# Kernel optimization log

Measured on AMD Instinct MI355X. Metric: run time of the kernel, lower is better.

The kernel has to match this reference:

```python
import jax, jax.numpy as jnp
import numpy as np

MAX_REL = 16  # max_relative_position (keys == values)


def _relative_positions(T, max_pos):
    r = jnp.arange(T)
    dist = r[None, :] - r[:, None]          # [T, T], k - q
    return jnp.clip(dist, -max_pos, max_pos) + max_pos


def setup_inputs() -> dict:
    key = jax.random.key(0)
    ks = jax.random.split(key, 5)
    B, H, T, D = 4, 16, 1024, 64
    V = 2 * MAX_REL + 1
    return {
        "q": jax.random.normal(ks[0], (B, H, T, D), jnp.float32),
        "k": jax.random.normal(ks[1], (B, H, T, D), jnp.float32),
        "v": jax.random.normal(ks[2], (B, H, T, D), jnp.float32),
        "emb_k": jax.random.normal(ks[3], (V, D), jnp.float32),
        "emb_v": jax.random.normal(ks[4], (V, D), jnp.float32),
    }


def reference(q, k, v, emb_k, emb_v):
    # q,k,v: [B,H,T,D]; emb_*: [2*MAX_REL+1, D]
    T = q.shape[2]
    D = k.shape[-1]
    rel_idx = _relative_positions(T, MAX_REL)          # [T,T]
    rel_k = emb_k[rel_idx]                             # [T,T,D]
    rel_v = emb_v[rel_idx]                             # [T,T,D]

    # content-content + content-position logits
    logits = jnp.einsum('bhtd,bhsd->bhts', q, k)
    logits = logits + jnp.einsum('bhtd,tsd->bhts', q, rel_k)
    logits = logits * (1.0 / jnp.sqrt(jnp.float32(D)))

    attn = jax.nn.softmax(logits, axis=-1)             # [B,H,T,T]
    out = jnp.einsum('bhts,bhsd->bhtd', attn, v)
    out = out + jnp.einsum('bhts,tsd->bhtd', attn, rel_v)
    return out, attn
```

## Files before the change

kernel.cpp:

```cpp
#include <hip/hip_runtime.h>
#include <hip/hip_bf16.h>

#define TT 1024
#define DD 64
#define MAXREL 16
#define NV 33
#define QBLK 16
#define SCALE 0.125f
#define BH 64

typedef short bf16x8 __attribute__((ext_vector_type(8)));
typedef short bf16x4 __attribute__((ext_vector_type(4)));
typedef float f32x4 __attribute__((ext_vector_type(4)));

#define SBAR() __builtin_amdgcn_sched_barrier(0)
#define WAITV(N)   __builtin_amdgcn_s_waitcnt(0x0F70 | (N))
#define WAITLGKM() __builtin_amdgcn_s_waitcnt(0xC07F)

static __device__ inline void gload16(const void* g, void* l) {
    __builtin_amdgcn_global_load_lds(
        (const __attribute__((address_space(1))) void*)g,
        (__attribute__((address_space(3))) void*)l, 16, 0, 0);
}

static __device__ inline short f2bf(float f) {
    __hip_bfloat16 h = __float2bfloat16(f);
    return *(short*)&h;
}
static __device__ inline float bf2f(short s) {
    union { unsigned u; float f; } x;
    x.u = ((unsigned)(unsigned short)s) << 16;
    return x.f;
}
static __device__ inline bf16x8 pack8(float4 a, float4 b) {
    bf16x8 r;
    r[0]=f2bf(a.x); r[1]=f2bf(a.y); r[2]=f2bf(a.z); r[3]=f2bf(a.w);
    r[4]=f2bf(b.x); r[5]=f2bf(b.y); r[6]=f2bf(b.z); r[7]=f2bf(b.w);
    return r;
}

__global__ __launch_bounds__(256)
void convk_kernel(const float* __restrict__ src, short* __restrict__ dst) {
    size_t i = (size_t)blockIdx.x * 256 + threadIdx.x;
    const float4* s = (const float4*)(src + i * 8);
    *(bf16x8*)(dst + i * 8) = pack8(s[0], s[1]);
}

__global__ __launch_bounds__(256)
void transv_kernel(const float* __restrict__ v, short* __restrict__ vt) {
    int bh = blockIdx.x >> 4;
    int st = blockIdx.x & 15;
    int wave = threadIdx.x >> 6, lane = threadIdx.x & 63;
    int s0 = st * 64 + wave * 16;
    const float* vp = v + ((size_t)bh * TT + s0) * DD + lane;
    bf16x8 lo, hi;
    #pragma unroll
    for (int e = 0; e < 8; ++e) lo[e] = f2bf(vp[(size_t)e * DD]);
    #pragma unroll
    for (int e = 0; e < 8; ++e) hi[e] = f2bf(vp[(size_t)(e + 8) * DD]);
    short* dp = vt + ((size_t)bh * DD + lane) * TT + s0;
    *(bf16x8*)dp = lo;
    *(bf16x8*)(dp + 8) = hi;
}

__global__ __launch_bounds__(256)
void relattn_kernel(const float* __restrict__ q_g,
                    const short* __restrict__ kb,
                    const short* __restrict__ vt,
                    const float* __restrict__ ek_g,
                    const float* __restrict__ ev_g,
                    float* __restrict__ out_g,
                    float* __restrict__ attn_g) {
    __shared__ __align__(16) char pbuf[QBLK * 2048];
    __shared__ __align__(16) char kstage[4 * 4096];
    __shared__ float qe_lds[QBLK * NV];
    __shared__ float w_lds[QBLK * NV];
    __shared__ float psum_lds[QBLK][4];
    __shared__ float psuf_lds[QBLK][4];
    __shared__ float pmid_lds[QBLK][4];
    __shared__ float inv_lds[QBLK];

    const int t    = threadIdx.x;
    const int bid  = blockIdx.x;
    const int wg   = ((bid & 7) << 9) | (bid >> 3);
    const int bh   = wg >> 6;
    const int q0   = (wg & 63) * QBLK;
    const int wave = t >> 6;
    const int lane = t & 63;
    const int lr   = lane & 15;
    const int akg  = lane >> 4;
    const int srl  = lane >> 3;
    const int sqg  = (lane & 7) ^ srl;

    const short* kgbase = kb + (size_t)bh * TT * DD;
    char* kst = kstage + wave * 4096;

    auto KSTAGE = [&](int B, int NT) {
        const int s0 = wave * 256 + NT * 16;
        gload16(kgbase + (size_t)(s0 + srl) * 64 + sqg * 8,     kst + B * 2048);
        gload16(kgbase + (size_t)(s0 + 8 + srl) * 64 + sqg * 8, kst + B * 2048 + 1024);
    };

    bf16x8 qF0, qF1;
    {
        const float* qp = q_g + ((size_t)bh * TT + q0 + lr) * DD + akg * 8;
        float4 a = *(const float4*)qp,        b = *(const float4*)(qp + 4);
        float4 c = *(const float4*)(qp + 32), d = *(const float4*)(qp + 36);
        qF0 = pack8(a, b); qF1 = pack8(c, d);
    }

    KSTAGE(0, 0); KSTAGE(1, 1);

    for (int i = t; i < QBLK * NV; i += 256) w_lds[i] = 0.f;
    if (wave < 3) {
        int v = wave * 16 + lr; if (v > 32) v = 32;
        const float* ep = ek_g + v * DD + akg * 8;
        float4 a = *(const float4*)ep,        b = *(const float4*)(ep + 4);
        float4 c = *(const float4*)(ep + 32), d = *(const float4*)(ep + 36);
        bf16x8 eF0 = pack8(a, b), eF1 = pack8(c, d);
        f32x4 qacc = {0.f, 0.f, 0.f, 0.f};
        qacc = __builtin_amdgcn_mfma_f32_16x16x32_bf16(eF0, qF0, qacc, 0, 0, 0);
        qacc = __builtin_amdgcn_mfma_f32_16x16x32_bf16(eF1, qF1, qacc, 0, 0, 0);
        #pragma unroll
        for (int j = 0; j < 4; ++j) {
            int vv = wave * 16 + akg * 4 + j;
            if (vv < NV) qe_lds[lr * NV + vv] = __expf(qacc[j] * SCALE);
        }
    }
    __syncthreads();

    {
        const int tq = q0 + lr;
        const int X  = (lr & 7) << 4;
        const float eqe_lo = qe_lds[lr * NV];
        const float eqe_hi = qe_lds[lr * NV + 32];
        float sum = 0.f, suff = 0.f, msum = 0.f;

        auto CVALU = [&](f32x4 acc, int nt) {
            const int sb = wave * 256 + nt * 16 + akg * 4;
            float ex0 = __expf(acc[0] * SCALE), ex1 = __expf(acc[1] * SCALE);
            float ex2 = __expf(acc[2] * SCALE), ex3 = __expf(acc[3] * SCALE);
            float e0, e1, e2, e3;
            if (sb >= tq + MAXREL) {
                e0 = ex0 * eqe_hi; e1 = ex1 * eqe_hi;
                e2 = ex2 * eqe_hi; e3 = ex3 * eqe_hi;
                float csum = (e0 + e1) + (e2 + e3);
                sum += csum; suff += csum;
            } else if (sb + 3 <= tq - MAXREL) {
                e0 = ex0 * eqe_lo; e1 = ex1 * eqe_lo;
                e2 = ex2 * eqe_lo; e3 = ex3 * eqe_lo;
                sum += (e0 + e1) + (e2 + e3);
            } else {
                float ee[4]; float exs[4] = {ex0, ex1, ex2, ex3};
                #pragma unroll
                for (int j = 0; j < 4; ++j) {
                    int dr = sb + j - tq;
                    int dc = dr < -MAXREL ? -MAXREL : (dr > MAXREL ? MAXREL : dr);
                    float v = exs[j] * qe_lds[lr * NV + dc + MAXREL];
                    ee[j] = v;
                    sum += v;
                    if (dr >= MAXREL) suff += v;
                    if (dr > -MAXREL && dr < MAXREL) {
                        w_lds[lr * NV + dr + MAXREL] = v;
                        msum += v;
                    }
                }
                e0 = ee[0]; e1 = ee[1]; e2 = ee[2]; e3 = ee[3];
            }
            bf16x4 p4;
            p4[0] = f2bf(e0); p4[1] = f2bf(e1);
            p4[2] = f2bf(e2); p4[3] = f2bf(e3);
            *(bf16x4*)(pbuf + lr * 2048 + ((2 * sb) ^ X)) = p4;
        };

        auto MFMA2 = [&](bf16x8 kf0, bf16x8 kf1) {
            f32x4 acc = {0.f, 0.f, 0.f, 0.f};
            acc = __builtin_amdgcn_mfma_f32_16x16x32_bf16(kf0, qF0, acc, 0, 0, 0);
            acc = __builtin_amdgcn_mfma_f32_16x16x32_bf16(kf1, qF1, acc, 0, 0, 0);
            return acc;
        };

        f32x4 aA, aB;
        #define CITER(B, NT, W, PF, AC, AP, NP) \
            WAITV(W); SBAR(); \
            { bf16x8 kf0 = *(const bf16x8*)(kst + (B)*2048 + lr*128 + ((((akg))  ^(lr&7)) << 4)); \
              bf16x8 kf1 = *(const bf16x8*)(kst + (B)*2048 + lr*128 + ((((akg)+4)^(lr&7)) << 4)); \
              if ((NP) >= 0) CVALU(AP, NP); \
              WAITLGKM(); SBAR(); \
              if (PF) KSTAGE((B), (NT) + 2); \
              AC = MFMA2(kf0, kf1); } \
            SBAR()
        CITER(0, 0, 2, 1, aA, aB, -1);
        CITER(1, 1, 2, 1, aB, aA,  0);
        CITER(0, 2, 2, 1, aA, aB,  1);
        CITER(1, 3, 2, 1, aB, aA,  2);
        CITER(0, 4, 2, 1, aA, aB,  3);
        CITER(1, 5, 2, 1, aB, aA,  4);
        CITER(0, 6, 2, 1, aA, aB,  5);
        CITER(1, 7, 2, 1, aB, aA,  6);
        CITER(0, 8, 2, 1, aA, aB,  7);
        CITER(1, 9, 2, 1, aB, aA,  8);
        CITER(0,10, 2, 1, aA, aB,  9);
        CITER(1,11, 2, 1, aB, aA, 10);
        CITER(0,12, 2, 1, aA, aB, 11);
        CITER(1,13, 2, 1, aB, aA, 12);
        CITER(0,14, 2, 0, aA, aB, 13);
        CITER(1,15, 0, 0, aB, aA, 14);
        CVALU(aB, 15);
        #undef CITER

        {
            WAITLGKM(); SBAR();
            const short* vgbase = vt + ((size_t)bh * DD + wave * 16) * TT;
            gload16(vgbase + (size_t)srl * TT + 0 * 64 + sqg * 8,       kst);
            gload16(vgbase + (size_t)(8 + srl) * TT + 0 * 64 + sqg * 8, kst + 1024);
            gload16(vgbase + (size_t)srl * TT + 1 * 64 + sqg * 8,       kst + 2048);
            gload16(vgbase + (size_t)(8 + srl) * TT + 1 * 64 + sqg * 8, kst + 3072);
        }

        sum  += __shfl_xor(sum, 16);  sum  += __shfl_xor(sum, 32);
        suff += __shfl_xor(suff, 16); suff += __shfl_xor(suff, 32);
        msum += __shfl_xor(msum, 16); msum += __shfl_xor(msum, 32);
        if (lane < 16) {
            psum_lds[lr][wave] = sum;
            psuf_lds[lr][wave] = suff;
            pmid_lds[lr][wave] = msum;
        }
    }
    __syncthreads();

    if (t < QBLK) {
        float s  = (psum_lds[t][0] + psum_lds[t][1]) + (psum_lds[t][2] + psum_lds[t][3]);
        float sf = (psuf_lds[t][0] + psuf_lds[t][1]) + (psuf_lds[t][2] + psuf_lds[t][3]);
        float sm = (pmid_lds[t][0] + pmid_lds[t][1]) + (pmid_lds[t][2] + pmid_lds[t][3]);
        inv_lds[t] = 1.0f / s;
        w_lds[t * NV]      = s - sf - sm;
        w_lds[t * NV + 32] = sf;
    }
    __syncthreads();

    {
        const int lc = lane & 15;
        const int dcol = wave * 16 + lc;
        const char* pb = pbuf + lc * 2048;
        const int X = (lc & 7) << 4;
        char* vst = kst;
        const short* vgbase = vt + ((size_t)bh * DD + wave * 16) * TT;
        f32x4 acc0 = {0.f, 0.f, 0.f, 0.f};
        f32x4 acc1 = {0.f, 0.f, 0.f, 0.f};

        auto VSTAGE = [&](int B, int S) {
            gload16(vgbase + (size_t)srl * TT + S * 64 + sqg * 8,       vst + B * 2048);
            gload16(vgbase + (size_t)(8 + srl) * TT + S * 64 + sqg * 8, vst + B * 2048 + 1024);
        };

        #define FITER(B, S, W, PF, AC) \
            WAITV(W); SBAR(); \
            { bf16x8 vf0 = *(const bf16x8*)(vst + (B)*2048 + lc*128 + ((((akg))  ^(lc&7)) << 4)); \
              bf16x8 vf1 = *(const bf16x8*)(vst + (B)*2048 + lc*128 + ((((akg)+4)^(lc&7)) << 4)); \
              bf16x8 a0 = *(const bf16x8*)(pb + (((2*(S))*64     + akg*16) ^ X)); \
              bf16x8 a1 = *(const bf16x8*)(pb + (((2*(S)+1)*64   + akg*16) ^ X)); \
              WAITLGKM(); SBAR(); \
              if (PF) VSTAGE((B), (S) + 2); \
              AC = __builtin_amdgcn_mfma_f32_16x16x32_bf16(a0, vf0, AC, 0, 0, 0); \
              AC = __builtin_amdgcn_mfma_f32_16x16x32_bf16(a1, vf1, AC, 0, 0, 0); } \
            SBAR()
        FITER(0, 0, 2, 1, acc0);  FITER(1, 1, 2, 1, acc1);
        FITER(0, 2, 2, 1, acc0);  FITER(1, 3, 2, 1, acc1);
        FITER(0, 4, 2, 1, acc0);  FITER(1, 5, 2, 1, acc1);
        FITER(0, 6, 2, 1, acc0);  FITER(1, 7, 2, 1, acc1);
        FITER(0, 8, 2, 1, acc0);  FITER(1, 9, 2, 1, acc1);
        FITER(0,10, 2, 1, acc0);  FITER(1,11, 2, 1, acc1);
        FITER(0,12, 2, 1, acc0);  FITER(1,13, 2, 1, acc1);
        FITER(0,14, 2, 0, acc0);  FITER(1,15, 0, 0, acc1);
        #undef FITER

        f32x4 acc;
        acc[0] = acc0[0] + acc1[0]; acc[1] = acc0[1] + acc1[1];
        acc[2] = acc0[2] + acc1[2]; acc[3] = acc0[3] + acc1[3];

        const int rb = akg * 4;
        float o0 = acc[0], o1 = acc[1], o2 = acc[2], o3 = acc[3];
        #pragma unroll 8
        for (int v = 0; v < NV; ++v) {
            float ev = ev_g[v * DD + dcol];
            o0 += w_lds[(rb + 0) * NV + v] * ev;
            o1 += w_lds[(rb + 1) * NV + v] * ev;
            o2 += w_lds[(rb + 2) * NV + v] * ev;
            o3 += w_lds[(rb + 3) * NV + v] * ev;
        }
        float* op = out_g + ((size_t)bh * TT + q0 + rb) * DD + dcol;
        op[0 * DD] = o0 * inv_lds[rb + 0];
        op[1 * DD] = o1 * inv_lds[rb + 1];
        op[2 * DD] = o2 * inv_lds[rb + 2];
        op[3 * DD] = o3 * inv_lds[rb + 3];
    }

    {
        float* ab = attn_g + ((size_t)bh * TT + q0) * TT;
        #pragma unroll
        for (int j = 0; j < 4; ++j) {
            const int r = wave * 4 + j;
            const float inv = inv_lds[r];
            const int X = (r & 7) << 4;
            #pragma unroll
            for (int i = 0; i < 4; ++i) {
                bf16x4 p4 = *(const bf16x4*)(pbuf + r * 2048 + ((8 * lane + 512 * i) ^ X));
                f32x4 o;
                o[0] = bf2f(p4[0]) * inv; o[1] = bf2f(p4[1]) * inv;
                o[2] = bf2f(p4[2]) * inv; o[3] = bf2f(p4[3]) * inv;
                __builtin_nontemporal_store(o, (f32x4*)(ab + (size_t)r * TT + lane * 4 + 256 * i));
            }
        }
    }
}

extern "C" void kernel_launch(void* const* d_in, const int* in_sizes, int n_in,
                              void* d_out, int out_size, void* d_ws, size_t ws_size,
                              hipStream_t stream) {
    const float* q  = (const float*)d_in[0];
    const float* k  = (const float*)d_in[1];
    const float* v  = (const float*)d_in[2];
    const float* ek = (const float*)d_in[3];
    const float* ev = (const float*)d_in[4];
    float* out  = (float*)d_out;
    float* attn = out + (size_t)BH * TT * DD;

    short* kbuf = (short*)d_ws;
    short* vtb  = kbuf + (size_t)BH * TT * DD;

    convk_kernel<<<dim3(2048), dim3(256), 0, stream>>>(k, kbuf);
    transv_kernel<<<dim3(1024), dim3(256), 0, stream>>>(v, vtb);
    relattn_kernel<<<dim3(4096), dim3(256), 0, stream>>>(q, kbuf, vtb, ek, ev, out, attn);
}
```

Before: 138.9 us.

## Fuse PV matmul into the QK loop with direct global V loads

Each wave now computes P·V partials for its own 256-key slice inside the QK loop, interleaved with the score MFMAs, reading V fragments directly from global memory instead of staging them through LDS in a separate phase. Partial outputs from the four waves are written to LDS and summed afterwards. This removes the separate serialized PV phase and its LDS staging pipeline. In exchange it adds unstaged global loads in the hot loop, a cross-wave reduction through LDS, and extra accumulator registers. It also depends on P being read back from pbuf within the same wave with no barrier in between.

```diff
diff --git a/kernel.cpp b/kernel.cpp
--- a/kernel.cpp
+++ b/kernel.cpp
@@ -128,6 +128,9 @@
         }
     }
     __syncthreads();
+
+    f32x4 acc0 = {0.f,0.f,0.f,0.f}, acc1 = {0.f,0.f,0.f,0.f};
+    f32x4 acc2 = {0.f,0.f,0.f,0.f}, acc3 = {0.f,0.f,0.f,0.f};
 
     {
         const int tq = q0 + lr;
@@ -180,42 +183,60 @@
             return acc;
         };
 
+        auto PV = [&](int S) {
+            bf16x8 pa = *(const bf16x8*)(pbuf + lr * 2048 +
+                                         ((wave * 512 + S * 64 + akg * 16) ^ X));
+            const short* vb = vt + ((size_t)bh * DD + lr) * TT + wave * 256 + S * 32 + akg * 8;
+            bf16x8 v0 = *(const bf16x8*)(vb);
+            bf16x8 v1 = *(const bf16x8*)(vb + 16 * TT);
+            bf16x8 v2 = *(const bf16x8*)(vb + 32 * TT);
+            bf16x8 v3 = *(const bf16x8*)(vb + 48 * TT);
+            acc0 = __builtin_amdgcn_mfma_f32_16x16x32_bf16(pa, v0, acc0, 0, 0, 0);
+            acc1 = __builtin_amdgcn_mfma_f32_16x16x32_bf16(pa, v1, acc1, 0, 0, 0);
+            acc2 = __builtin_amdgcn_mfma_f32_16x16x32_bf16(pa, v2, acc2, 0, 0, 0);
+            acc3 = __builtin_amdgcn_mfma_f32_16x16x32_bf16(pa, v3, acc3, 0, 0, 0);
+        };
+
         f32x4 aA, aB;
-        #define CITER(B, NT, W, PF, AC, AP, NP) \
+        #define CITER(B, NT, W, PF, AC, AP, NP, PVS) \
             WAITV(W); SBAR(); \
             { bf16x8 kf0 = *(const bf16x8*)(kst + (B)*2048 + lr*128 + ((((akg))  ^(lr&7)) << 4)); \
               bf16x8 kf1 = *(const bf16x8*)(kst + (B)*2048 + lr*128 + ((((akg)+4)^(lr&7)) << 4)); \
               if ((NP) >= 0) CVALU(AP, NP); \
               WAITLGKM(); SBAR(); \
               if (PF) KSTAGE((B), (NT) + 2); \
-              AC = MFMA2(kf0, kf1); } \
+              AC = MFMA2(kf0, kf1); \
+              if ((PVS) >= 0) PV(PVS); } \
             SBAR()
-        CITER(0, 0, 2, 1, aA, aB, -1);
-        CITER(1, 1, 2, 1, aB, aA,  0);
-        CITER(0, 2, 2, 1, aA, aB,  1);
-        CITER(1, 3, 2, 1, aB, aA,  2);
-        CITER(0, 4, 2, 1, aA, aB,  3);
-        CITER(1, 5, 2, 1, aB, aA,  4);
-        CITER(0, 6, 2, 1, aA, aB,  5);
-        CITER(1, 7, 2, 1, aB, aA,  6);
-        CITER(0, 8, 2, 1, aA, aB,  7);
-        CITER(1, 9, 2, 1, aB, aA,  8);
-        CITER(0,10, 2, 1, aA, aB,  9);
-        CITER(1,11, 2, 1, aB, aA, 10);
-        CITER(0,12, 2, 1, aA, aB, 11);
-        CITER(1,13, 2, 1, aB, aA, 12);
-        CITER(0,14, 2, 0, aA, aB, 13);
-        CITER(1,15, 0, 0, aB, aA, 14);
+        CITER(0, 0, 2, 1, aA, aB, -1, -1);
+        CITER(1, 1, 2, 1, aB, aA,  0, -1);
+        CITER(0, 2, 2, 1, aA, aB,  1, -1);
+        CITER(1, 3, 2, 1, aB, aA,  2,  0);
+        CITER(0, 4, 2, 1, aA, aB,  3, -1);
+        CITER(1, 5, 2, 1, aB, aA,  4,  1);
+        CITER(0, 6, 2, 1, aA, aB,  5, -1);
+        CITER(1, 7, 2, 1, aB, aA,  6,  2);
+        CITER(0, 8, 2, 1, aA, aB,  7, -1);
+        CITER(1, 9, 2, 1, aB, aA,  8,  3);
+        CITER(0,10, 2, 1, aA, aB,  9, -1);
+        CITER(1,11, 2, 1, aB, aA, 10,  4);
+        CITER(0,12, 2, 1, aA, aB, 11, -1);
+        CITER(1,13, 2, 1, aB, aA, 12,  5);
+        CITER(0,14, 2, 0, aA, aB, 13, -1);
+        CITER(1,15, 0, 0, aB, aA, 14,  6);
         CVALU(aB, 15);
+        PV(7);
         #undef CITER
 
         {
-            WAITLGKM(); SBAR();
-            const short* vgbase = vt + ((size_t)bh * DD + wave * 16) * TT;
-            gload16(vgbase + (size_t)srl * TT + 0 * 64 + sqg * 8,       kst);
-            gload16(vgbase + (size_t)(8 + srl) * TT + 0 * 64 + sqg * 8, kst + 1024);
-            gload16(vgbase + (size_t)srl * TT + 1 * 64 + sqg * 8,       kst + 2048);
-            gload16(vgbase + (size_t)(8 + srl) * TT + 1 * 64 + sqg * 8, kst + 3072);
+            float* pw = (float*)kstage + wave * 1024;
+            #define PSTORE(A, DT) \
+                pw[(akg * 4 + 0) * 64 + (DT)*16 + lr] = A[0]; \
+                pw[(akg * 4 + 1) * 64 + (DT)*16 + lr] = A[1]; \
+                pw[(akg * 4 + 2) * 64 + (DT)*16 + lr] = A[2]; \
+                pw[(akg * 4 + 3) * 64 + (DT)*16 + lr] = A[3]
+            PSTORE(acc0, 0); PSTORE(acc1, 1); PSTORE(acc2, 2); PSTORE(acc3, 3);
+            #undef PSTORE
         }
 
         sum  += __shfl_xor(sum, 16);  sum  += __shfl_xor(sum, 32);
@@ -242,45 +263,19 @@
     {
         const int lc = lane & 15;
         const int dcol = wave * 16 + lc;
-        const char* pb = pbuf + lc * 2048;
-        const int X = (lc & 7) << 4;
-        char* vst = kst;
-        const short* vgbase = vt + ((size_t)bh * DD + wave * 16) * TT;
-        f32x4 acc0 = {0.f, 0.f, 0.f, 0.f};
-        f32x4 acc1 = {0.f, 0.f, 0.f, 0.f};
-
-        auto VSTAGE = [&](int B, int S) {
-            gload16(vgbase + (size_t)srl * TT + S * 64 + sqg * 8,       vst + B * 2048);
-            gload16(vgbase + (size_t)(8 + srl) * TT + S * 64 + sqg * 8, vst + B * 2048 + 1024);
-        };
-
-        #define FITER(B, S, W, PF, AC) \
-            WAITV(W); SBAR(); \
-            { bf16x8 vf0 = *(const bf16x8*)(vst + (B)*2048 + lc*128 + ((((akg))  ^(lc&7)) << 4)); \
-              bf16x8 vf1 = *(const bf16x8*)(vst + (B)*2048 + lc*128 + ((((akg)+4)^(lc&7)) << 4)); \
-              bf16x8 a0 = *(const bf16x8*)(pb + (((2*(S))*64     + akg*16) ^ X)); \
-              bf16x8 a1 = *(const bf16x8*)(pb + (((2*(S)+1)*64   + akg*16) ^ X)); \
-              WAITLGKM(); SBAR(); \
-              if (PF) VSTAGE((B), (S) + 2); \
-              AC = __builtin_amdgcn_mfma_f32_16x16x32_bf16(a0, vf0, AC, 0, 0, 0); \
-              AC = __builtin_amdgcn_mfma_f32_16x16x32_bf16(a1, vf1, AC, 0, 0, 0); } \
-            SBAR()
-        FITER(0, 0, 2, 1, acc0);  FITER(1, 1, 2, 1, acc1);
-        FITER(0, 2, 2, 1, acc0);  FITER(1, 3, 2, 1, acc1);
-        FITER(0, 4, 2, 1, acc0);  FITER(1, 5, 2, 1, acc1);
-        FITER(0, 6, 2, 1, acc0);  FITER(1, 7, 2, 1, acc1);
-        FITER(0, 8, 2, 1, acc0);  FITER(1, 9, 2, 1, acc1);
-        FITER(0,10, 2, 1, acc0);  FITER(1,11, 2, 1, acc1);
-        FITER(0,12, 2, 1, acc0);  FITER(1,13, 2, 1, acc1);
-        FITER(0,14, 2, 0, acc0);  FITER(1,15, 0, 0, acc1);
-        #undef FITER
-
-        f32x4 acc;
-        acc[0] = acc0[0] + acc1[0]; acc[1] = acc0[1] + acc1[1];
-        acc[2] = acc0[2] + acc1[2]; acc[3] = acc0[3] + acc1[3];
-
         const int rb = akg * 4;
-        float o0 = acc[0], o1 = acc[1], o2 = acc[2], o3 = acc[3];
+        const float* pr = (const float*)kstage;
+        float o0, o1, o2, o3;
+        {
+            const float* p0 = pr + (rb + 0) * 64 + dcol;
+            const float* p1 = pr + (rb + 1) * 64 + dcol;
+            const float* p2 = pr + (rb + 2) * 64 + dcol;
+            const float* p3 = pr + (rb + 3) * 64 + dcol;
+            o0 = (p0[0] + p0[1024]) + (p0[2048] + p0[3072]);
+            o1 = (p1[0] + p1[1024]) + (p1[2048] + p1[3072]);
+            o2 = (p2[0] + p2[1024]) + (p2[2048] + p2[3072]);
+            o3 = (p3[0] + p3[1024]) + (p3[2048] + p3[3072]);
+        }
         #pragma unroll 8
         for (int v = 0; v < NV; ++v) {
             float ev = ev_g[v * DD + dcol];
```

Measured after the change: 146.7 us. +5.6%, slower.

## Split relattn work across eight waves instead of four per block

Applied to the files above, without the earlier changes.

Doubles the block to 512 threads. Each wave now scans half as many key tiles (128 keys instead of 256). In the PV phase two waves split the key range for each 16-column output tile and combine their partial sums through a small LDS buffer, and the attention writeback is spread across all eight waves. The aim is more latency hiding and parallelism per query block. In exchange it needs more LDS for staging, an extra block barrier, and it may reduce how many blocks fit on a CU.

```diff
diff --git a/kernel.cpp b/kernel.cpp
--- a/kernel.cpp
+++ b/kernel.cpp
@@ -63,7 +63,7 @@
     *(bf16x8*)(dp + 8) = hi;
 }
 
-__global__ __launch_bounds__(256)
+__global__ __launch_bounds__(512)
 void relattn_kernel(const float* __restrict__ q_g,
                     const short* __restrict__ kb,
                     const short* __restrict__ vt,
@@ -72,12 +72,13 @@
                     float* __restrict__ out_g,
                     float* __restrict__ attn_g) {
     __shared__ __align__(16) char pbuf[QBLK * 2048];
-    __shared__ __align__(16) char kstage[4 * 4096];
+    __shared__ __align__(16) char kstage[8 * 4096];
+    __shared__ float pair_lds[4][16][16];
     __shared__ float qe_lds[QBLK * NV];
     __shared__ float w_lds[QBLK * NV];
-    __shared__ float psum_lds[QBLK][4];
-    __shared__ float psuf_lds[QBLK][4];
-    __shared__ float pmid_lds[QBLK][4];
+    __shared__ float psum_lds[QBLK][8];
+    __shared__ float psuf_lds[QBLK][8];
+    __shared__ float pmid_lds[QBLK][8];
     __shared__ float inv_lds[QBLK];
 
     const int t    = threadIdx.x;
@@ -85,7 +86,7 @@
     const int wg   = ((bid & 7) << 9) | (bid >> 3);
     const int bh   = wg >> 6;
     const int q0   = (wg & 63) * QBLK;
-    const int wave = t >> 6;
+    const int w    = t >> 6;
     const int lane = t & 63;
     const int lr   = lane & 15;
     const int akg  = lane >> 4;
@@ -93,10 +94,10 @@
     const int sqg  = (lane & 7) ^ srl;
 
     const short* kgbase = kb + (size_t)bh * TT * DD;
-    char* kst = kstage + wave * 4096;
+    char* kst = kstage + w * 4096;
 
     auto KSTAGE = [&](int B, int NT) {
-        const int s0 = wave * 256 + NT * 16;
+        const int s0 = w * 128 + NT * 16;
         gload16(kgbase + (size_t)(s0 + srl) * 64 + sqg * 8,     kst + B * 2048);
         gload16(kgbase + (size_t)(s0 + 8 + srl) * 64 + sqg * 8, kst + B * 2048 + 1024);
     };
@@ -111,9 +112,9 @@
 
     KSTAGE(0, 0); KSTAGE(1, 1);
 
-    for (int i = t; i < QBLK * NV; i += 256) w_lds[i] = 0.f;
-    if (wave < 3) {
-        int v = wave * 16 + lr; if (v > 32) v = 32;
+    for (int i = t; i < QBLK * NV; i += 512) w_lds[i] = 0.f;
+    if (w < 3) {
+        int v = w * 16 + lr; if (v > 32) v = 32;
         const float* ep = ek_g + v * DD + akg * 8;
         float4 a = *(const float4*)ep,        b = *(const float4*)(ep + 4);
         float4 c = *(const float4*)(ep + 32), d = *(const float4*)(ep + 36);
@@ -123,7 +124,7 @@
         qacc = __builtin_amdgcn_mfma_f32_16x16x32_bf16(eF1, qF1, qacc, 0, 0, 0);
         #pragma unroll
         for (int j = 0; j < 4; ++j) {
-            int vv = wave * 16 + akg * 4 + j;
+            int vv = w * 16 + akg * 4 + j;
             if (vv < NV) qe_lds[lr * NV + vv] = __expf(qacc[j] * SCALE);
         }
     }
@@ -137,7 +138,7 @@
         float sum = 0.f, suff = 0.f, msum = 0.f;
 
         auto CVALU = [&](f32x4 acc, int nt) {
-            const int sb = wave * 256 + nt * 16 + akg * 4;
+            const int sb = w * 128 + nt * 16 + akg * 4;
             float ex0 = __expf(acc[0] * SCALE), ex1 = __expf(acc[1] * SCALE);
             float ex2 = __expf(acc[2] * SCALE), ex3 = __expf(acc[3] * SCALE);
             float e0, e1, e2, e3;
@@ -196,43 +197,40 @@
         CITER(1, 3, 2, 1, aB, aA,  2);
         CITER(0, 4, 2, 1, aA, aB,  3);
         CITER(1, 5, 2, 1, aB, aA,  4);
-        CITER(0, 6, 2, 1, aA, aB,  5);
-        CITER(1, 7, 2, 1, aB, aA,  6);
-        CITER(0, 8, 2, 1, aA, aB,  7);
-        CITER(1, 9, 2, 1, aB, aA,  8);
-        CITER(0,10, 2, 1, aA, aB,  9);
-        CITER(1,11, 2, 1, aB, aA, 10);
-        CITER(0,12, 2, 1, aA, aB, 11);
-        CITER(1,13, 2, 1, aB, aA, 12);
-        CITER(0,14, 2, 0, aA, aB, 13);
-        CITER(1,15, 0, 0, aB, aA, 14);
-        CVALU(aB, 15);
+        CITER(0, 6, 2, 0, aA, aB,  5);
+        CITER(1, 7, 0, 0, aB, aA,  6);
+        CVALU(aB, 7);
         #undef CITER
 
         {
             WAITLGKM(); SBAR();
-            const short* vgbase = vt + ((size_t)bh * DD + wave * 16) * TT;
-            gload16(vgbase + (size_t)srl * TT + 0 * 64 + sqg * 8,       kst);
-            gload16(vgbase + (size_t)(8 + srl) * TT + 0 * 64 + sqg * 8, kst + 1024);
-            gload16(vgbase + (size_t)srl * TT + 1 * 64 + sqg * 8,       kst + 2048);
-            gload16(vgbase + (size_t)(8 + srl) * TT + 1 * 64 + sqg * 8, kst + 3072);
+            const short* vgbase = vt + ((size_t)bh * DD + (w & 3) * 16) * TT;
+            const int S0 = (w >> 2) * 8;
+            gload16(vgbase + (size_t)srl * TT + S0 * 64 + sqg * 8,           kst);
+            gload16(vgbase + (size_t)(8 + srl) * TT + S0 * 64 + sqg * 8,     kst + 1024);
+            gload16(vgbase + (size_t)srl * TT + (S0 + 1) * 64 + sqg * 8,     kst + 2048);
+            gload16(vgbase + (size_t)(8 + srl) * TT + (S0 + 1) * 64 + sqg * 8, kst + 3072);
         }
 
         sum  += __shfl_xor(sum, 16);  sum  += __shfl_xor(sum, 32);
         suff += __shfl_xor(suff, 16); suff += __shfl_xor(suff, 32);
         msum += __shfl_xor(msum, 16); msum += __shfl_xor(msum, 32);
         if (lane < 16) {
-            psum_lds[lr][wave] = sum;
-            psuf_lds[lr][wave] = suff;
-            pmid_lds[lr][wave] = msum;
+            psum_lds[lr][w] = sum;
+            psuf_lds[lr][w] = suff;
+            pmid_lds[lr][w] = msum;
         }
     }
     __syncthreads();
 
     if (t < QBLK) {
-        float s  = (psum_lds[t][0] + psum_lds[t][1]) + (psum_lds[t][2] + psum_lds[t][3]);
-        float sf = (psuf_lds[t][0] + psuf_lds[t][1]) + (psuf_lds[t][2] + psuf_lds[t][3]);
-        float sm = (pmid_lds[t][0] + pmid_lds[t][1]) + (pmid_lds[t][2] + pmid_lds[t][3]);
+        float s = 0.f, sf = 0.f, sm = 0.f;
+        #pragma unroll
+        for (int i = 0; i < 8; ++i) {
+            s  += psum_lds[t][i];
+            sf += psuf_lds[t][i];
+            sm += pmid_lds[t][i];
+        }
         inv_lds[t] = 1.0f / s;
         w_lds[t * NV]      = s - sf - sm;
         w_lds[t * NV + 32] = sf;
@@ -240,12 +238,15 @@
     __syncthreads();
 
     {
+        const int dt = w & 3;
+        const int sh = w >> 2;
+        const int S0 = sh * 8;
         const int lc = lane & 15;
-        const int dcol = wave * 16 + lc;
+        const int dcol = dt * 16 + lc;
         const char* pb = pbuf + lc * 2048;
         const int X = (lc & 7) << 4;
         char* vst = kst;
-        const short* vgbase = vt + ((size_t)bh * DD + wave * 16) * TT;
+        const short* vgbase = vt + ((size_t)bh * DD + dt * 16) * TT;
         f32x4 acc0 = {0.f, 0.f, 0.f, 0.f};
         f32x4 acc1 = {0.f, 0.f, 0.f, 0.f};
 
@@ -265,42 +266,50 @@
               AC = __builtin_amdgcn_mfma_f32_16x16x32_bf16(a0, vf0, AC, 0, 0, 0); \
               AC = __builtin_amdgcn_mfma_f32_16x16x32_bf16(a1, vf1, AC, 0, 0, 0); } \
             SBAR()
-        FITER(0, 0, 2, 1, acc0);  FITER(1, 1, 2, 1, acc1);
-        FITER(0, 2, 2, 1, acc0);  FITER(1, 3, 2, 1, acc1);
-        FITER(0, 4, 2, 1, acc0);  FITER(1, 5, 2, 1, acc1);
-        FITER(0, 6, 2, 1, acc0);  FITER(1, 7, 2, 1, acc1);
-        FITER(0, 8, 2, 1, acc0);  FITER(1, 9, 2, 1, acc1);
-        FITER(0,10, 2, 1, acc0);  FITER(1,11, 2, 1, acc1);
-        FITER(0,12, 2, 1, acc0);  FITER(1,13, 2, 1, acc1);
-        FITER(0,14, 2, 0, acc0);  FITER(1,15, 0, 0, acc1);
+        FITER(0, S0 + 0, 2, 1, acc0);  FITER(1, S0 + 1, 2, 1, acc1);
+        FITER(0, S0 + 2, 2, 1, acc0);  FITER(1, S0 + 3, 2, 1, acc1);
+        FITER(0, S0 + 4, 2, 1, acc0);  FITER(1, S0 + 5, 2, 1, acc1);
+        FITER(0, S0 + 6, 2, 0, acc0);  FITER(1, S0 + 7, 0, 0, acc1);
         #undef FITER
 
         f32x4 acc;
         acc[0] = acc0[0] + acc1[0]; acc[1] = acc0[1] + acc1[1];
         acc[2] = acc0[2] + acc1[2]; acc[3] = acc0[3] + acc1[3];
 
-        const int rb = akg * 4;
-        float o0 = acc[0], o1 = acc[1], o2 = acc[2], o3 = acc[3];
-        #pragma unroll 8
-        for (int v = 0; v < NV; ++v) {
-            float ev = ev_g[v * DD + dcol];
-            o0 += w_lds[(rb + 0) * NV + v] * ev;
-            o1 += w_lds[(rb + 1) * NV + v] * ev;
-            o2 += w_lds[(rb + 2) * NV + v] * ev;
-            o3 += w_lds[(rb + 3) * NV + v] * ev;
-        }
-        float* op = out_g + ((size_t)bh * TT + q0 + rb) * DD + dcol;
-        op[0 * DD] = o0 * inv_lds[rb + 0];
-        op[1 * DD] = o1 * inv_lds[rb + 1];
-        op[2 * DD] = o2 * inv_lds[rb + 2];
-        op[3 * DD] = o3 * inv_lds[rb + 3];
+        if (sh == 1) {
+            #pragma unroll
+            for (int j = 0; j < 4; ++j)
+                pair_lds[dt][akg * 4 + j][lc] = acc[j];
+        }
+        __syncthreads();
+
+        if (sh == 0) {
+            const int rb = akg * 4;
+            float o0 = acc[0] + pair_lds[dt][rb + 0][lc];
+            float o1 = acc[1] + pair_lds[dt][rb + 1][lc];
+            float o2 = acc[2] + pair_lds[dt][rb + 2][lc];
+            float o3 = acc[3] + pair_lds[dt][rb + 3][lc];
+            #pragma unroll 8
+            for (int v = 0; v < NV; ++v) {
+                float ev = ev_g[v * DD + dcol];
+                o0 += w_lds[(rb + 0) * NV + v] * ev;
+                o1 += w_lds[(rb + 1) * NV + v] * ev;
+                o2 += w_lds[(rb + 2) * NV + v] * ev;
+                o3 += w_lds[(rb + 3) * NV + v] * ev;
+            }
+            float* op = out_g + ((size_t)bh * TT + q0 + rb) * DD + dcol;
+            op[0 * DD] = o0 * inv_lds[rb + 0];
+            op[1 * DD] = o1 * inv_lds[rb + 1];
+            op[2 * DD] = o2 * inv_lds[rb + 2];
+            op[3 * DD] = o3 * inv_lds[rb + 3];
+        }
     }
 
     {
         float* ab = attn_g + ((size_t)bh * TT + q0) * TT;
         #pragma unroll
-        for (int j = 0; j < 4; ++j) {
-            const int r = wave * 4 + j;
+        for (int j = 0; j < 2; ++j) {
+            const int r = w * 2 + j;
             const float inv = inv_lds[r];
             const int X = (r & 7) << 4;
             #pragma unroll
@@ -331,5 +340,5 @@
 
     convk_kernel<<<dim3(2048), dim3(256), 0, stream>>>(k, kbuf);
     transv_kernel<<<dim3(1024), dim3(256), 0, stream>>>(v, vtb);
-    relattn_kernel<<<dim3(4096), dim3(256), 0, stream>>>(q, kbuf, vtb, ek, ev, out, attn);
-}
+    relattn_kernel<<<dim3(4096), dim3(512), 0, stream>>>(q, kbuf, vtb, ek, ev, out, attn);
+}
```

Result: faster. 118.9 us, median of 2 (-14.4%).
